# Kernel optimization log

Measured on AMD Instinct MI355X. Metric: run time of the kernel, lower is better.

Reference implementation:

```python
import jax, jax.numpy as jnp
import numpy as np

ROUTINGS = 3

def _squash_size1(s):
    # Faithful to squash(tensor, dim=-1) applied on a size-1 last dim:
    # squared_norm degenerates to elementwise s**2.
    sq = s * s
    return (sq / (1.0 + sq)) * s / jnp.sqrt(sq + 1e-9)

def setup_inputs() -> dict:
    key = jax.random.key(0)
    k1, k2 = jax.random.split(key)
    B, I, Din = 16, 1152, 16
    N, D = 32, 64
    inputs = jax.random.normal(k1, (B, I, Din), dtype=jnp.float32)
    W = jax.random.normal(k2, (1, N, I, D, Din), dtype=jnp.float32)
    return {"inputs": inputs, "W": W}

def reference(inputs, W):
    # inputs: [B, I, Din]; W: [1, N, I, D, Din]
    # torch: matmul(W, inputs.unsqueeze(1).unsqueeze(4)) -> [B,N,I,D,1]; drop trailing 1.
    x_hat = jnp.einsum('nidk,bik->bnid', W[0], inputs)  # [B, N, I, D]
    b = jnp.zeros_like(x_hat)                            # [B, N, I, D] (quirk: carries D axis)
    outputs = None
    for i in range(ROUTINGS):
        c = jax.nn.softmax(b, axis=2)                    # softmax over input capsules
        s = jnp.sum(c * x_hat, axis=2)                   # [B, N, D]
        outputs = _squash_size1(s)                       # elementwise squash (size-1 dim quirk)
        if i < ROUTINGS - 1:
            # (inputs_hat * outputs).sum(dim=-1) over size-1 dim == elementwise product
            b = b + x_hat * outputs[:, :, None, :]
    return outputs[..., None]                            # [B, N, D, 1] (after squeeze(2))
```

## Files before the change

### kernel.cpp

```cpp
#include <hip/hip_runtime.h>
#include <hip/hip_bf16.h>
#include <math.h>

#define B_   16
#define N_   32
#define I_   1152
#define DIN  16
#define D_   64
#define TI   16
#define IB   (I_/TI)
#define IC   16
#define BND  (B_*N_*D_)

#if __has_builtin(__builtin_amdgcn_exp2f)
#define EXP2(x) __builtin_amdgcn_exp2f(x)
#else
#define EXP2(x) exp2f(x)
#endif

#define LOG2E 1.4426950408889634f

typedef __attribute__((ext_vector_type(8))) short short8v;
typedef __attribute__((ext_vector_type(4))) float f32x4;
typedef __attribute__((ext_vector_type(4))) unsigned int u32x4;
typedef __attribute__((ext_vector_type(2))) unsigned int u32x2;

__device__ __forceinline__ float squash1(float s) {
    float sq = s * s;
    return (sq / (1.0f + sq)) * s * rsqrtf(sq + 1e-9f);
}
__device__ __forceinline__ unsigned int bfh(float v) {
    return (unsigned int)__builtin_bit_cast(unsigned short, __float2bfloat16(v));
}
__device__ __forceinline__ float bff(unsigned int hi16) {
    return __builtin_bit_cast(float, hi16 << 16);
}
__device__ __forceinline__ unsigned int cvtpk(float a, float b) {
    unsigned int r;
    asm("v_cvt_pk_bf16_f32 %0, %1, %2" : "=v"(r) : "v"(a), "v"(b));
    return r;
}

__global__ __launch_bounds__(256, 3) void k_xhat(const float* __restrict__ inp,
                                                 const float* __restrict__ W,
                                                 unsigned short* __restrict__ xh2,
                                                 float* __restrict__ part) {
    __shared__ __align__(16) unsigned short xs[4096];
    const int bx = blockIdx.x;
    const int n  = bx / IB;
    const int ib = bx % IB;
    const int i0 = ib * TI;
    const int t  = threadIdx.x;
    const int l  = t & 63;
    const int mt = t >> 6;
    const int row = l & 15;
    const int ko  = (l >> 4) & 1;
    const bool loHalf = (l >= 32);

    #pragma unroll
    for (int rep = 0; rep < 2; ++rep) {
        int s   = rep * 256 + t;
        int bb  = s >> 5;
        int il  = (s >> 1) & 15;
        int sko = s & 1;
        const float* src = inp + (size_t)bb * (I_ * DIN) + (size_t)(i0 + il) * DIN + sko * 8;
        f32x4 a0 = *(const f32x4*)src;
        f32x4 a1 = *(const f32x4*)(src + 4);
        u32x4 p;
        p.x = cvtpk(a0.x, a0.y);
        p.y = cvtpk(a0.z, a0.w);
        p.z = cvtpk(a1.x, a1.y);
        p.w = cvtpk(a1.z, a1.w);
        int base = (bb * 512 + il * 32 + sko * 16) ^ ((bb & 7) << 4);
        *(u32x4*)((char*)xs + base) = p;
    }
    __syncthreads();

    const float* wb = W + ((size_t)(n * I_ + i0) * 64 + mt * 16 + row) * 16 + ko * 8;

    unsigned int pk[TI * 2];
    f32x4 s0v = {0.f, 0.f, 0.f, 0.f};

#define LOADG(DST, C) {                                                        \
        _Pragma("unroll")                                                      \
        for (int j = 0; j < 4; ++j) {                                          \
            const f32x4* p = (const f32x4*)(wb + (size_t)((C) * 4 + j) * 1024);\
            DST[2 * j] = p[0]; DST[2 * j + 1] = p[1];                          \
        } }

#define COMPG(SRC, C) {                                                        \
        _Pragma("unroll")                                                      \
        for (int j = 0; j < 4; ++j) {                                          \
            const int i = (C) * 4 + j;                                         \
            f32x4 w0 = SRC[2 * j], w1 = SRC[2 * j + 1];                        \
            u32x4 b0 = __builtin_bit_cast(u32x4, w0);                          \
            u32x4 b1 = __builtin_bit_cast(u32x4, w1);                          \
            u32x4 ah, al;                                                      \
            ah.x = __builtin_amdgcn_perm(b0.y, b0.x, 0x07060302u);             \
            ah.y = __builtin_amdgcn_perm(b0.w, b0.z, 0x07060302u);             \
            ah.z = __builtin_amdgcn_perm(b1.y, b1.x, 0x07060302u);             \
            ah.w = __builtin_amdgcn_perm(b1.w, b1.z, 0x07060302u);             \
            float r0 = w0.x - __builtin_bit_cast(float, b0.x & 0xffff0000u);   \
            float r1 = w0.y - __builtin_bit_cast(float, b0.y & 0xffff0000u);   \
            float r2 = w0.z - __builtin_bit_cast(float, b0.z & 0xffff0000u);   \
            float r3 = w0.w - __builtin_bit_cast(float, b0.w & 0xffff0000u);   \
            float r4 = w1.x - __builtin_bit_cast(float, b1.x & 0xffff0000u);   \
            float r5 = w1.y - __builtin_bit_cast(float, b1.y & 0xffff0000u);   \
            float r6 = w1.z - __builtin_bit_cast(float, b1.z & 0xffff0000u);   \
            float r7 = w1.w - __builtin_bit_cast(float, b1.w & 0xffff0000u);   \
            al.x = cvtpk(r0, r1);                                              \
            al.y = cvtpk(r2, r3);                                              \
            al.z = cvtpk(r4, r5);                                              \
            al.w = cvtpk(r6, r7);                                              \
            u32x4 aw;                                                          \
            aw.x = loHalf ? al.x : ah.x;                                       \
            aw.y = loHalf ? al.y : ah.y;                                       \
            aw.z = loHalf ? al.z : ah.z;                                       \
            aw.w = loHalf ? al.w : ah.w;                                       \
            short8v afrag = __builtin_bit_cast(short8v, aw);                   \
            int xaddr = ((l & 15) * 512 + i * 32 + ko * 16) ^ (((l & 15) & 7) << 4); \
            short8v bfrag = *(const short8v*)((const char*)xs + xaddr);        \
            f32x4 acc = __builtin_amdgcn_mfma_f32_16x16x32_bf16(               \
                afrag, bfrag, (f32x4){0.f, 0.f, 0.f, 0.f}, 0, 0, 0);           \
            s0v += acc;                                                        \
            pk[i * 2]     = cvtpk(acc[0], acc[1]);                             \
            pk[i * 2 + 1] = cvtpk(acc[2], acc[3]);                             \
        } }

    f32x4 wA[8], wB[8];
    LOADG(wA, 0)
    LOADG(wB, 1)
    COMPG(wA, 0)
    LOADG(wA, 2)
    COMPG(wB, 1)
    LOADG(wB, 3)
    COMPG(wA, 2)
    COMPG(wB, 3)
#undef LOADG
#undef COMPG

    size_t pidx = (((size_t)ib * B_ + (l & 15)) * N_ + n) * 64 + mt * 16 + (l >> 4) * 4;
    *(f32x4*)(part + pidx) = s0v;

    #pragma unroll
    for (int i = 0; i < TI; ++i) {
        u32x2 v;
        v.x = pk[i * 2];
        v.y = pk[i * 2 + 1];
        size_t off = (size_t)(n * I_ + i0 + i) * 1024 + (size_t)t * 4;
        *reinterpret_cast<u32x2*>(xh2 + off) = v;
    }
}

__global__ __launch_bounds__(256) void k_out0(const float* __restrict__ part,
                                              float* __restrict__ coef) {
    const int t = blockIdx.x * 256 + threadIdx.x;
    float s = 0.0f;
    for (int j = 0; j < IB; ++j) s += part[(size_t)j * BND + t];
    s *= (1.0f / (float)I_);
    coef[t] = squash1(s);
}

__global__ __launch_bounds__(256) void k_rpart(const unsigned short* __restrict__ xh2,
                                               const float* __restrict__ coef,
                                               float* __restrict__ part2) {
    const int bx = blockIdx.x;
    const int n  = bx >> 4;
    const int ic = bx & 15;
    const int t  = threadIdx.x;
    const int b  = t & 15;
    const int d0 = (t >> 4) * 4;

    const unsigned short* base = xh2 + ((size_t)n * I_ + (size_t)ic * (I_ / IC)) * 1024
                               + (size_t)t * 4;
    f32x4 c4 = *(const f32x4*)(coef + ((size_t)b * N_ + n) * 64 + d0);
    float c2[4] = {c4.x * LOG2E, c4.y * LOG2E, c4.z * LOG2E, c4.w * LOG2E};
    float z[4] = {0, 0, 0, 0}, a[4] = {0, 0, 0, 0};

    #pragma unroll 8
    for (int i = 0; i < I_ / IC; ++i) {
        u32x2 u = *(const u32x2*)(base + (size_t)i * 1024);
        unsigned short s4[4] = {(unsigned short)(u.x & 0xffffu), (unsigned short)(u.x >> 16),
                                (unsigned short)(u.y & 0xffffu), (unsigned short)(u.y >> 16)};
        #pragma unroll
        for (int j = 0; j < 4; ++j) {
            float x = bff(s4[j]);
            float e = EXP2(x * c2[j]);
            z[j] += e;
            a[j] = fmaf(e, x, a[j]);
        }
    }

    size_t pidx = ((((size_t)ic * N_ + n) * 16 + b) * 64 + d0) * 2;
    f32x4 v0 = {z[0], a[0], z[1], a[1]};
    f32x4 v1 = {z[2], a[2], z[3], a[3]};
    *(f32x4*)(part2 + pidx)     = v0;
    *(f32x4*)(part2 + pidx + 4) = v1;
}

__global__ __launch_bounds__(256) void k_rfin(const float* __restrict__ part2,
                                              const float* __restrict__ coefIn,
                                              float* __restrict__ outp,
                                              int final_) {
    const int gid = blockIdx.x * 256 + threadIdx.x;
    float Z = 0.0f, A = 0.0f;
    #pragma unroll
    for (int ic = 0; ic < IC; ++ic) {
        const float* p = part2 + ((size_t)ic * BND + gid) * 2;
        Z += p[0];
        A += p[1];
    }
    const int d = gid & 63, b = (gid >> 6) & 15, n = gid >> 10;
    const int ci = (b * N_ + n) * D_ + d;
    float o = squash1(A / Z);
    outp[ci] = final_ ? o : (coefIn[ci] + o);
}

extern "C" void kernel_launch(void* const* d_in, const int* in_sizes, int n_in,
                              void* d_out, int out_size, void* d_ws, size_t ws_size,
                              hipStream_t stream) {
    const float* inp = (const float*)d_in[0];
    const float* W   = (const float*)d_in[1];
    float* out = (float*)d_out;

    unsigned short* xh2 = (unsigned short*)d_ws;
    float* part  = (float*)((char*)d_ws + 75497472);
    float* part2 = (float*)((char*)d_ws + 84934656);
    float* coef  = (float*)((char*)d_ws + 89128960);

    k_xhat<<<dim3(N_ * IB), dim3(256), 0, stream>>>(inp, W, xh2, part);
    k_out0<<<dim3(BND / 256), dim3(256), 0, stream>>>(part, coef);
    k_rpart<<<dim3(N_ * IC), dim3(256), 0, stream>>>(xh2, coef, part2);
    k_rfin <<<dim3(BND / 256), dim3(256), 0, stream>>>(part2, coef, coef, 0);
    k_rpart<<<dim3(N_ * IC), dim3(256), 0, stream>>>(xh2, coef, part2);
    k_rfin <<<dim3(BND / 256), dim3(256), 0, stream>>>(part2, coef, out, 1);
}
```

Before: 75.79 us.

## Fuse capsule routing into one cooperative kernel keeping x_hat in registers

Replaces the six-kernel pipeline with a single cooperative kernel of 512 blocks. Each block computes its slice of x_hat with MFMA, keeps it packed as bf16 in registers (144 uint per thread), and runs all routing passes locally, using grid-wide syncs to reduce the small partial sums. This removes the global write and re-read of the roughly 75 MB x_hat tensor and the launch gaps between kernels. The cost is heavy register pressure and three grid barriers. The old multi-kernel path stays as a fallback when occupancy or the cooperative launch fails.

```diff
diff --git a/kernel.cpp b/kernel.cpp
--- a/kernel.cpp
+++ b/kernel.cpp
@@ -1,12 +1,17 @@
 #include <hip/hip_runtime.h>
+#include <hip/hip_cooperative_groups.h>
 #include <hip/hip_bf16.h>
 #include <math.h>
+
+namespace cg = cooperative_groups;
 
 #define B_   16
 #define N_   32
 #define I_   1152
 #define DIN  16
 #define D_   64
+#define JC   16
+#define IPC  72
 #define TI   16
 #define IB   (I_/TI)
 #define IC   16
@@ -39,6 +44,168 @@
     unsigned int r;
     asm("v_cvt_pk_bf16_f32 %0, %1, %2" : "=v"(r) : "v"(a), "v"(b));
     return r;
+}
+
+__global__ __launch_bounds__(256, 2) void k_caps(const float* __restrict__ inp,
+                                                 const float* __restrict__ W,
+                                                 float* __restrict__ outp,
+                                                 float* __restrict__ p0,
+                                                 float* __restrict__ za1,
+                                                 float* __restrict__ za2) {
+    __shared__ __align__(16) unsigned short xs[IPC * 256];
+
+    cg::grid_group grid = cg::this_grid();
+
+    const int bid = blockIdx.x;
+    const int n  = bid >> 4;
+    const int jc = bid & 15;
+    const int t  = threadIdx.x;
+    const int l  = t & 63;
+    const int w  = t >> 6;
+    const int b  = l & 15;
+    const int dg = l >> 4;
+    const int ko = dg & 1;
+    const bool loHalf = (l >= 32);
+    const int d0 = w * 16 + dg * 4;
+
+    for (int rep = 0; rep < 5; ++rep) {
+        int slot = rep * 256 + t;
+        if (slot < IPC * 16) {
+            int il = slot >> 4, bb = slot & 15;
+            const float* src = inp + (size_t)bb * (I_ * DIN) + (size_t)(jc * IPC + il) * DIN;
+            f32x4 a0 = *(const f32x4*)src;
+            f32x4 a1 = *(const f32x4*)(src + 4);
+            f32x4 a2 = *(const f32x4*)(src + 8);
+            f32x4 a3 = *(const f32x4*)(src + 12);
+            u32x4 q0, q1;
+            q0.x = (bfh(a0.y) << 16) | bfh(a0.x);
+            q0.y = (bfh(a0.w) << 16) | bfh(a0.z);
+            q0.z = (bfh(a1.y) << 16) | bfh(a1.x);
+            q0.w = (bfh(a1.w) << 16) | bfh(a1.z);
+            q1.x = (bfh(a2.y) << 16) | bfh(a2.x);
+            q1.y = (bfh(a2.w) << 16) | bfh(a2.z);
+            q1.z = (bfh(a3.y) << 16) | bfh(a3.x);
+            q1.w = (bfh(a3.w) << 16) | bfh(a3.z);
+            *(u32x4*)(xs + il * 256 + bb * 8)       = q0;
+            *(u32x4*)(xs + il * 256 + 128 + bb * 8) = q1;
+        }
+    }
+    __syncthreads();
+
+    const float* wb = W + ((size_t)(n * I_ + jc * IPC) * D_ + w * 16 + b) * DIN + ko * 8;
+
+    unsigned int pk[IPC * 2];
+    f32x4 s0v = {0.f, 0.f, 0.f, 0.f};
+
+    #pragma unroll
+    for (int c = 0; c < IPC / 4; ++c) {
+        f32x4 wv[8];
+        #pragma unroll
+        for (int j = 0; j < 4; ++j) {
+            const f32x4* p = (const f32x4*)(wb + (size_t)(c * 4 + j) * 1024);
+            wv[2 * j] = p[0]; wv[2 * j + 1] = p[1];
+        }
+        #pragma unroll
+        for (int j = 0; j < 4; ++j) {
+            const int i = c * 4 + j;
+            short8v bfrag = *(const short8v*)(xs + i * 256 + ko * 128 + b * 8);
+            short8v afrag;
+            #pragma unroll
+            for (int q = 0; q < 8; ++q) {
+                float wq = wv[2 * j + (q >> 2)][q & 3];
+                unsigned int hi = bfh(wq);
+                unsigned int lo = bfh(wq - bff(hi));
+                afrag[q] = (short)(loHalf ? lo : hi);
+            }
+            f32x4 acc = __builtin_amdgcn_mfma_f32_16x16x32_bf16(
+                afrag, bfrag, (f32x4){0.f, 0.f, 0.f, 0.f}, 0, 0, 0);
+            s0v += acc;
+            pk[i * 2]     = (bfh(acc[1]) << 16) | bfh(acc[0]);
+            pk[i * 2 + 1] = (bfh(acc[3]) << 16) | bfh(acc[2]);
+        }
+    }
+
+    *(f32x4*)(p0 + (size_t)(n * JC + jc) * 1024 + b * 64 + d0) = s0v;
+    __threadfence();
+    grid.sync();
+
+#define ROUTE_PASS(C2, ZZ, AA)                                                  \
+    _Pragma("unroll")                                                           \
+    for (int iw = 0; iw < IPC; ++iw) {                                          \
+        unsigned int u0 = pk[iw * 2], u1 = pk[iw * 2 + 1];                      \
+        float x0 = __builtin_bit_cast(float, u0 << 16);                         \
+        float x1 = __builtin_bit_cast(float, u0 & 0xffff0000u);                 \
+        float x2 = __builtin_bit_cast(float, u1 << 16);                         \
+        float x3 = __builtin_bit_cast(float, u1 & 0xffff0000u);                 \
+        float e0 = EXP2(x0 * C2[0]); ZZ[0] += e0; AA[0] = fmaf(e0, x0, AA[0]);  \
+        float e1 = EXP2(x1 * C2[1]); ZZ[1] += e1; AA[1] = fmaf(e1, x1, AA[1]);  \
+        float e2 = EXP2(x2 * C2[2]); ZZ[2] += e2; AA[2] = fmaf(e2, x2, AA[2]);  \
+        float e3 = EXP2(x3 * C2[3]); ZZ[3] += e3; AA[3] = fmaf(e3, x3, AA[3]);  \
+    }
+
+    float coef0[4], c2[4];
+    {
+        f32x4 s = {0.f, 0.f, 0.f, 0.f};
+        #pragma unroll
+        for (int j = 0; j < JC; ++j)
+            s += *(const f32x4*)(p0 + (size_t)(n * JC + j) * 1024 + b * 64 + d0);
+        #pragma unroll
+        for (int r = 0; r < 4; ++r) {
+            coef0[r] = squash1(s[r] * (1.0f / (float)I_));
+            c2[r] = coef0[r] * LOG2E;
+        }
+    }
+    float z[4] = {0, 0, 0, 0}, a[4] = {0, 0, 0, 0};
+    ROUTE_PASS(c2, z, a)
+    {
+        size_t base = ((size_t)(n * JC + jc) * 1024 + b * 64 + d0) * 2;
+        *(f32x4*)(za1 + base)     = (f32x4){z[0], a[0], z[1], a[1]};
+        *(f32x4*)(za1 + base + 4) = (f32x4){z[2], a[2], z[3], a[3]};
+    }
+    __threadfence();
+    grid.sync();
+
+    float cn2[4];
+    {
+        f32x4 Z = {0.f, 0.f, 0.f, 0.f}, A = {0.f, 0.f, 0.f, 0.f};
+        #pragma unroll
+        for (int j = 0; j < JC; ++j) {
+            size_t base = ((size_t)(n * JC + j) * 1024 + b * 64 + d0) * 2;
+            f32x4 v0 = *(const f32x4*)(za1 + base);
+            f32x4 v1 = *(const f32x4*)(za1 + base + 4);
+            Z += (f32x4){v0[0], v0[2], v1[0], v1[2]};
+            A += (f32x4){v0[1], v0[3], v1[1], v1[3]};
+        }
+        #pragma unroll
+        for (int r = 0; r < 4; ++r)
+            cn2[r] = (coef0[r] + squash1(A[r] / Z[r])) * LOG2E;
+    }
+    float z2[4] = {0, 0, 0, 0}, a2[4] = {0, 0, 0, 0};
+    ROUTE_PASS(cn2, z2, a2)
+    {
+        size_t base = ((size_t)(n * JC + jc) * 1024 + b * 64 + d0) * 2;
+        *(f32x4*)(za2 + base)     = (f32x4){z2[0], a2[0], z2[1], a2[1]};
+        *(f32x4*)(za2 + base + 4) = (f32x4){z2[2], a2[2], z2[3], a2[3]};
+    }
+    __threadfence();
+    grid.sync();
+
+    if (jc == 0) {
+        f32x4 Z = {0.f, 0.f, 0.f, 0.f}, A = {0.f, 0.f, 0.f, 0.f};
+        #pragma unroll
+        for (int j = 0; j < JC; ++j) {
+            size_t base = ((size_t)(n * JC + j) * 1024 + b * 64 + d0) * 2;
+            f32x4 v0 = *(const f32x4*)(za2 + base);
+            f32x4 v1 = *(const f32x4*)(za2 + base + 4);
+            Z += (f32x4){v0[0], v0[2], v1[0], v1[2]};
+            A += (f32x4){v0[1], v0[3], v1[1], v1[3]};
+        }
+        f32x4 o;
+        #pragma unroll
+        for (int r = 0; r < 4; ++r) o[r] = squash1(A[r] / Z[r]);
+        *(f32x4*)(outp + (size_t)b * (N_ * D_) + n * 64 + d0) = o;
+    }
+#undef ROUTE_PASS
 }
 
 __global__ __launch_bounds__(256, 3) void k_xhat(const float* __restrict__ inp,
@@ -223,15 +390,34 @@
     const float* W   = (const float*)d_in[1];
     float* out = (float*)d_out;
 
-    unsigned short* xh2 = (unsigned short*)d_ws;
-    float* part  = (float*)((char*)d_ws + 75497472);
-    float* part2 = (float*)((char*)d_ws + 84934656);
-    float* coef  = (float*)((char*)d_ws + 89128960);
-
-    k_xhat<<<dim3(N_ * IB), dim3(256), 0, stream>>>(inp, W, xh2, part);
-    k_out0<<<dim3(BND / 256), dim3(256), 0, stream>>>(part, coef);
-    k_rpart<<<dim3(N_ * IC), dim3(256), 0, stream>>>(xh2, coef, part2);
-    k_rfin <<<dim3(BND / 256), dim3(256), 0, stream>>>(part2, coef, coef, 0);
-    k_rpart<<<dim3(N_ * IC), dim3(256), 0, stream>>>(xh2, coef, part2);
-    k_rfin <<<dim3(BND / 256), dim3(256), 0, stream>>>(part2, coef, out, 1);
-}
+    float* p0  = (float*)d_ws;
+    float* za1 = (float*)((char*)d_ws + (2u << 20));
+    float* za2 = (float*)((char*)d_ws + (6u << 20));
+
+    int occ = 0;
+    hipError_t qe = hipOccupancyMaxActiveBlocksPerMultiprocessor(
+        &occ, (const void*)k_caps, 256, 0);
+    bool coop = (qe == hipSuccess && occ >= 2);
+
+    if (coop) {
+        void* args[] = {(void*)&inp, (void*)&W, (void*)&out,
+                        (void*)&p0, (void*)&za1, (void*)&za2};
+        hipError_t le = hipLaunchCooperativeKernel((void*)k_caps, dim3(N_ * JC),
+                                                   dim3(256), args, 0, stream);
+        if (le != hipSuccess) coop = false;
+    }
+
+    if (!coop) {
+        unsigned short* xh2 = (unsigned short*)((char*)d_ws + (12u << 20));
+        float* part  = (float*)((char*)d_ws + (12u << 20) + 75497472);
+        float* part2 = (float*)((char*)d_ws + (12u << 20) + 84934656);
+        float* coefb = (float*)((char*)d_ws + (12u << 20) + 89128960);
+
+        k_xhat<<<dim3(N_ * IB), dim3(256), 0, stream>>>(inp, W, xh2, part);
+        k_out0<<<dim3(BND / 256), dim3(256), 0, stream>>>(part, coefb);
+        k_rpart<<<dim3(N_ * IC), dim3(256), 0, stream>>>(xh2, coefb, part2);
+        k_rfin <<<dim3(BND / 256), dim3(256), 0, stream>>>(part2, coefb, coefb, 0);
+        k_rpart<<<dim3(N_ * IC), dim3(256), 0, stream>>>(xh2, coefb, part2);
+        k_rfin <<<dim3(BND / 256), dim3(256), 0, stream>>>(part2, coefb, out, 1);
+    }
+}
```

Measured after the change: 75.80 us. No clear change (+0.0%).
